# Kernel optimization log

Hardware: AMD Instinct MI355X
Metric: run time of the kernel (lower is better)

Reference implementation:

```python
import jax, jax.numpy as jnp
import numpy as np

EDGE_DROPOUT_RATE = 0.5  # RGCNEncoder edge_dropout_rate
DROPOUT_KEY = 42         # fixed key standing in for the encoder's dropout_key


def setup_inputs() -> dict:
    key = jax.random.key(0)
    ks = jax.random.split(key, 6)
    N, R, E, D, B, BI, BO = 100000, 16, 50000, 500, 100, 5, 5
    x = 0.01 * jax.random.normal(ks[0], (N, D), dtype=jnp.float32)  # pre_transform, normal() init (stddev=0.01)
    # block-decomposed relation weights: R relations x 100 blocks of 5x5
    w_rel1 = jax.random.normal(ks[1], (R, B, BI, BO), dtype=jnp.float32) / np.sqrt(BI)
    w_self1 = jax.random.normal(ks[2], (D, D), dtype=jnp.float32) / np.sqrt(D)
    w_rel2 = jax.random.normal(ks[3], (R, B, BI, BO), dtype=jnp.float32) / np.sqrt(BI)
    w_self2 = jax.random.normal(ks[4], (D, D), dtype=jnp.float32) / np.sqrt(D)
    edge_type_idcs = jax.random.randint(ks[5], (R, 2, E), 0, N, dtype=jnp.int32)
    edge_masks = jnp.ones((R, E), dtype=bool)
    return {"x": x, "w_rel1": w_rel1, "w_self1": w_self1,
            "w_rel2": w_rel2, "w_self2": w_self2,
            "edge_type_idcs": edge_type_idcs, "edge_masks": edge_masks}


def _rgcn_layer(h, w_rel, w_self, edge_type_idcs, edge_mask_f):
    """One block-decomposed RGCNConv with per-relation-node normalization + self loop."""
    N = h.shape[0]
    R, B, BI, BO = w_rel.shape
    Dout = B * BO
    out = h @ w_self  # self-connection
    for r in range(R):  # small fixed set of relations
        src = edge_type_idcs[r, 0]
        dst = edge_type_idcs[r, 1]
        mr = edge_mask_f[r]                              # [E]
        E = src.shape[0]
        hs = h[src].reshape(E, B, BI)                    # gather + split into blocks
        msg = jnp.einsum('ebi,bio->ebo', hs, w_rel[r]).reshape(E, Dout)
        msg = msg * mr[:, None]                          # masked (incl. edge dropout)
        agg = jax.ops.segment_sum(msg, dst, num_segments=N)   # [N, Dout]
        cnt = jax.ops.segment_sum(mr, dst, num_segments=N)    # per-relation in-degree
        out = out + agg / jnp.maximum(cnt, 1.0)[:, None]
    return jax.nn.relu(out)


def reference(x, w_rel1, w_self1, w_rel2, w_self2, edge_type_idcs, edge_masks):
    # edge dropout (all_data.dropout): keep each edge with prob 1 - rate
    keep = jax.random.bernoulli(jax.random.key(DROPOUT_KEY), 1.0 - EDGE_DROPOUT_RATE, edge_masks.shape)
    mask_f = (edge_masks & keep).astype(x.dtype)
    h = _rgcn_layer(x, w_rel1, w_self1, edge_type_idcs, mask_f)
    h = _rgcn_layer(h, w_rel2, w_self2, edge_type_idcs, mask_f)
    return h
```

## Files before the change

kernel.cpp:

```cpp
#include <hip/hip_runtime.h>
#include <hip/hip_bf16.h>
#include <stdint.h>

#define N_NODES 100000
#define N_REL   16
#define N_EDGE  50000
#define DIM     500
#define TOT_E   (N_REL * N_EDGE)
#define CNT_N   (N_REL * N_NODES)

#define INV_OFF    0ull
#define DEG_OFF    6400000ull
#define ROW_OFF    6800000ull
#define SCANP_OFF  7201000ull
#define CURS_OFF   7210000ull
#define ELIST_OFF  7610000ull
#define WB1_OFF    14020000ull
#define WB2_OFF    14550000ull
#define H1_OFF     15080000ull
#define WEXP1_OFF  115080000ull
#define WEXP2_OFF  115240000ull

typedef __attribute__((ext_vector_type(8))) short bf16x8;
typedef __attribute__((ext_vector_type(4))) float f32x4;

__device__ __forceinline__ uint32_t rotl32(uint32_t x, int d) {
    return (x << d) | (x >> (32 - d));
}
__device__ __forceinline__ bool edge_keep(uint32_t j) {
    uint32_t x0 = 0u, x1 = j;
    const uint32_t ks0 = 0u, ks1 = 42u, ks2 = 0u ^ 42u ^ 0x1BD11BDAu;
    const int RA[4] = {13, 15, 26, 6};
    const int RB[4] = {17, 29, 16, 24};
    x0 += ks0; x1 += ks1;
#pragma unroll
    for (int i = 0; i < 4; i++) { x0 += x1; x1 = rotl32(x1, RA[i]); x1 ^= x0; }
    x0 += ks1; x1 += ks2 + 1u;
#pragma unroll
    for (int i = 0; i < 4; i++) { x0 += x1; x1 = rotl32(x1, RB[i]); x1 ^= x0; }
    x0 += ks2; x1 += ks0 + 2u;
#pragma unroll
    for (int i = 0; i < 4; i++) { x0 += x1; x1 = rotl32(x1, RA[i]); x1 ^= x0; }
    x0 += ks0; x1 += ks1 + 3u;
#pragma unroll
    for (int i = 0; i < 4; i++) { x0 += x1; x1 = rotl32(x1, RB[i]); x1 ^= x0; }
    x0 += ks1; x1 += ks2 + 4u;
#pragma unroll
    for (int i = 0; i < 4; i++) { x0 += x1; x1 = rotl32(x1, RA[i]); x1 ^= x0; }
    x0 += ks2; x1 += ks0 + 5u;
    return ((x0 ^ x1) >> 31) == 0u;
}

__device__ __forceinline__ uint16_t f2bf(float f) {
    uint32_t u = __float_as_uint(f);
    u += 0x7FFFu + ((u >> 16) & 1u);
    return (uint16_t)(u >> 16);
}
__device__ __forceinline__ float bf2f(uint16_t v) {
    return __uint_as_float((uint32_t)v << 16);
}

__global__ __launch_bounds__(256) void zero_kernel(uint32_t* __restrict__ p, int n) {
    int t = blockIdx.x * blockDim.x + threadIdx.x;
    if (t < n) p[t] = 0u;
}

__global__ __launch_bounds__(256) void count_kernel(
        const int* __restrict__ eidx, uint32_t* __restrict__ cnt,
        uint32_t* __restrict__ deg) {
    int tid = blockIdx.x * blockDim.x + threadIdx.x;
    if (tid >= TOT_E) return;
    if (edge_keep((uint32_t)tid)) {
        int r = tid / N_EDGE;
        int e = tid - r * N_EDGE;
        int dst = eidx[(r * 2 + 1) * N_EDGE + e];
        atomicAdd(&cnt[r * N_NODES + dst], 1u);
        atomicAdd(&deg[dst], 1u);
    }
}

__global__ __launch_bounds__(256) void inv_kernel(uint32_t* __restrict__ cnt_u,
                                                  float* __restrict__ inv) {
    int t = blockIdx.x * blockDim.x + threadIdx.x;
    if (t < CNT_N) {
        float c = (float)cnt_u[t];
        inv[t] = 1.0f / fmaxf(c, 1.0f);
    }
}

__global__ __launch_bounds__(256) void scan1_kernel(
        const uint32_t* __restrict__ deg, uint32_t* __restrict__ rowptr,
        uint32_t* __restrict__ scanp) {
    __shared__ uint32_t sh[256];
    int b = blockIdx.x, t = threadIdx.x;
    int base = b * 1024 + t * 4;
    uint32_t x[4];
#pragma unroll
    for (int i = 0; i < 4; i++) x[i] = (base + i < N_NODES) ? deg[base + i] : 0u;
    uint32_t s = x[0] + x[1] + x[2] + x[3];
    sh[t] = s; __syncthreads();
    for (int off = 1; off < 256; off <<= 1) {
        uint32_t v = (t >= off) ? sh[t - off] : 0u;
        __syncthreads();
        sh[t] += v;
        __syncthreads();
    }
    uint32_t run = sh[t] - s;
    if (t == 255) scanp[b] = sh[255];
#pragma unroll
    for (int i = 0; i < 4; i++) {
        if (base + i < N_NODES) rowptr[base + i] = run;
        run += x[i];
    }
}

__global__ __launch_bounds__(128) void scan2_kernel(
        uint32_t* __restrict__ scanp, uint32_t* __restrict__ rowptr, int nb) {
    __shared__ uint32_t sh[128];
    int t = threadIdx.x;
    uint32_t v = (t < nb) ? scanp[t] : 0u;
    sh[t] = v; __syncthreads();
    for (int off = 1; off < 128; off <<= 1) {
        uint32_t u = (t >= off) ? sh[t - off] : 0u;
        __syncthreads();
        sh[t] += u;
        __syncthreads();
    }
    if (t < nb) scanp[t] = sh[t] - v;
    if (t == 127) rowptr[N_NODES] = sh[127];
}

__global__ __launch_bounds__(256) void scan3_kernel(
        uint32_t* __restrict__ rowptr, const uint32_t* __restrict__ scanp,
        uint32_t* __restrict__ curs) {
    int b = blockIdx.x, t = threadIdx.x;
    int base = b * 1024 + t * 4;
    uint32_t off = scanp[b];
#pragma unroll
    for (int i = 0; i < 4; i++) {
        int idx = base + i;
        if (idx < N_NODES) {
            uint32_t v = rowptr[idx] + off;
            rowptr[idx] = v;
            curs[idx] = v;
        }
    }
}

__global__ __launch_bounds__(256) void scatter_kernel(
        const int* __restrict__ eidx, const float* __restrict__ inv,
        uint32_t* __restrict__ curs, uint2* __restrict__ elist2) {
    int tid = blockIdx.x * blockDim.x + threadIdx.x;
    if (tid >= TOT_E) return;
    if (edge_keep((uint32_t)tid)) {
        int r = tid / N_EDGE;
        int e = tid - r * N_EDGE;
        int src = eidx[(r * 2 + 0) * N_EDGE + e];
        int dst = eidx[(r * 2 + 1) * N_EDGE + e];
        uint32_t pos = atomicAdd(&curs[dst], 1u);
        uint2 rec;
        rec.x = (uint32_t)src | ((uint32_t)r << 20);
        rec.y = __float_as_uint(inv[r * N_NODES + dst]);
        elist2[pos] = rec;
    }
}

__global__ __launch_bounds__(256) void conv_x_kernel(
        const float4* __restrict__ in, ushort4* __restrict__ outp, int n4) {
    int t = blockIdx.x * blockDim.x + threadIdx.x;
    if (t >= n4) return;
    float4 v = in[t];
    ushort4 o;
    o.x = f2bf(v.x); o.y = f2bf(v.y); o.z = f2bf(v.z); o.w = f2bf(v.w);
    outp[t] = o;
}

__global__ __launch_bounds__(256) void conv_w_kernel(
        const float* __restrict__ W, uint16_t* __restrict__ Bt) {
    int idx = blockIdx.x * 256 + threadIdx.x;
    int n = idx >> 9, k = idx & 511;
    float v = (n < DIM && k < DIM) ? W[k * DIM + n] : 0.f;
    Bt[idx] = f2bf(v);
}

__global__ __launch_bounds__(256) void conv_wexp_kernel(
        const float* __restrict__ W, float* __restrict__ wexp) {
    int idx = blockIdx.x * 256 + threadIdx.x;
    if (idx >= N_REL * 5 * DIM) return;
    int r = idx / (5 * DIM);
    int rem = idx - r * 5 * DIM;
    int i = rem / DIM;
    int j = rem - i * DIM;
    wexp[idx] = W[r * 2500 + (j / 5) * 25 + i * 5 + (j % 5)];
}

__global__ __launch_bounds__(256) void gemm_mfma128_kernel(
        const uint16_t* __restrict__ A, const uint16_t* __restrict__ Bt,
        float* __restrict__ C, int M) {
    __shared__ uint16_t As[128][72];
    __shared__ uint16_t Bs[128][72];
    int m0 = blockIdx.x * 128;
    int n0 = blockIdx.y * 128;
    int t = threadIdx.x;
    int wave = t >> 6, lane = t & 63;
    int wm = wave >> 1, wn = wave & 1;
    f32x4 acc[4][4] = {};

    for (int k0 = 0; k0 < 512; k0 += 64) {
#pragma unroll
        for (int i = 0; i < 4; i++) {
            int c = t * 4 + i;
            int row = c >> 3;
            int col = (c & 7) * 8;
            int gm = m0 + row, gk = k0 + col;
            uint16_t* dst = &As[row][col];
            if (gm < M && gk + 7 < DIM) {
                *(bf16x8*)dst = *(const bf16x8*)&A[(size_t)gm * DIM + gk];
            } else {
#pragma unroll
                for (int q = 0; q < 8; q++)
                    dst[q] = (gm < M && gk + q < DIM) ? A[(size_t)gm * DIM + gk + q]
                                                      : (uint16_t)0;
            }
            *(bf16x8*)&Bs[row][col] =
                *(const bf16x8*)&Bt[(size_t)(n0 + row) * 512 + k0 + col];
        }
        __syncthreads();

        int ks = (lane >> 4) * 8;
        int rl = lane & 15;
        bf16x8 af[4][2], bfr[4][2];
#pragma unroll
        for (int mt = 0; mt < 4; mt++) {
            af[mt][0] = *(const bf16x8*)&As[wm * 64 + mt * 16 + rl][ks];
            af[mt][1] = *(const bf16x8*)&As[wm * 64 + mt * 16 + rl][32 + ks];
        }
#pragma unroll
        for (int nt = 0; nt < 4; nt++) {
            bfr[nt][0] = *(const bf16x8*)&Bs[wn * 64 + nt * 16 + rl][ks];
            bfr[nt][1] = *(const bf16x8*)&Bs[wn * 64 + nt * 16 + rl][32 + ks];
        }
#pragma unroll
        for (int mt = 0; mt < 4; mt++)
#pragma unroll
            for (int nt = 0; nt < 4; nt++) {
                acc[mt][nt] = __builtin_amdgcn_mfma_f32_16x16x32_bf16(
                    af[mt][0], bfr[nt][0], acc[mt][nt], 0, 0, 0);
                acc[mt][nt] = __builtin_amdgcn_mfma_f32_16x16x32_bf16(
                    af[mt][1], bfr[nt][1], acc[mt][nt], 0, 0, 0);
            }
        __syncthreads();
    }

    int cl = lane & 15;
    int rq = (lane >> 4) << 2;
#pragma unroll
    for (int mt = 0; mt < 4; mt++) {
        int rbase = m0 + wm * 64 + mt * 16 + rq;
#pragma unroll
        for (int nt = 0; nt < 4; nt++) {
            int col = n0 + wn * 64 + nt * 16 + cl;
            if (col < DIM) {
#pragma unroll
                for (int q = 0; q < 4; q++) {
                    int rr = rbase + q;
                    if (rr < M) C[(size_t)rr * DIM + col] = acc[mt][nt][q];
                }
            }
        }
    }
}

template <bool BF16H, bool OUT_BF16>
__global__ __launch_bounds__(256) void gather_kernel(
        const void* __restrict__ h, const float* __restrict__ wexp,
        const uint2* __restrict__ elist2, const uint32_t* __restrict__ rowptr,
        const float* __restrict__ self_in, float* __restrict__ out_f32,
        uint16_t* __restrict__ out_bf16) {
    int n = blockIdx.x;
    int wv = threadIdx.x >> 6, l = threadIdx.x & 63;
    const int D0 = wv * 125;
    const int j0 = l, j1 = l + 64;
    const bool has1 = (j1 < 125);
    const int b0 = j0 / 5;
    const int b1 = j1 / 5;

    __shared__ float hsb[4][2][128];

    long ob = (long)n * DIM + D0;
    float self0 = self_in[ob + j0];
    float self1 = has1 ? self_in[ob + j1] : 0.f;

    uint32_t s = rowptr[n], e = rowptr[n + 1];
    float a0 = 0.f, a1 = 0.f;

    for (uint32_t p = s; p < e; p += 4) {
        const int k = (int)min(4u, e - p);
        uint2 rec[4];
#pragma unroll
        for (int i = 0; i < 4; i++) {
            if (i < k) rec[i] = elist2[p + i];
        }
        float v0[4], v1[4];
#pragma unroll
        for (int i = 0; i < 4; i++) {
            if (i < k) {
                uint32_t src = rec[i].x & 0xFFFFFu;
                if constexpr (BF16H) {
                    const uint16_t* row = (const uint16_t*)h + (size_t)src * DIM + D0;
                    v0[i] = bf2f(row[j0]);
                    v1[i] = has1 ? bf2f(row[j1]) : 0.f;
                } else {
                    const float* row = (const float*)h + (size_t)src * DIM + D0;
                    v0[i] = row[j0];
                    v1[i] = has1 ? row[j1] : 0.f;
                }
            }
        }
#pragma unroll
        for (int i = 0; i < 4; i++) {
            if (i < k) {
                float* hs = hsb[wv][i & 1];
                hs[j0] = v0[i];
                if (has1) hs[j1] = v1[i];
                uint32_t rl = rec[i].x >> 20;
                float inv = __uint_as_float(rec[i].y);
                const float* wbase = wexp + (size_t)rl * (5 * DIM) + D0;
                float w0[5];
#pragma unroll
                for (int q = 0; q < 5; q++) w0[q] = wbase[q * DIM + j0];
                const float* hp0 = hs + b0 * 5;
                float d0 = hp0[0] * w0[0] + hp0[1] * w0[1] + hp0[2] * w0[2]
                         + hp0[3] * w0[3] + hp0[4] * w0[4];
                a0 = fmaf(inv, d0, a0);
                if (has1) {
                    float w1[5];
#pragma unroll
                    for (int q = 0; q < 5; q++) w1[q] = wbase[q * DIM + j1];
                    const float* hp1 = hs + b1 * 5;
                    float d1 = hp1[0] * w1[0] + hp1[1] * w1[1] + hp1[2] * w1[2]
                             + hp1[3] * w1[3] + hp1[4] * w1[4];
                    a1 = fmaf(inv, d1, a1);
                }
            }
        }
    }

    {
        float v = fmaxf(self0 + a0, 0.f);
        if (OUT_BF16) out_bf16[ob + j0] = f2bf(v);
        else          out_f32[ob + j0] = v;
    }
    if (has1) {
        float v = fmaxf(self1 + a1, 0.f);
        if (OUT_BF16) out_bf16[ob + j1] = f2bf(v);
        else          out_f32[ob + j1] = v;
    }
}

extern "C" void kernel_launch(void* const* d_in, const int* in_sizes, int n_in,
                              void* d_out, int out_size, void* d_ws, size_t ws_size,
                              hipStream_t stream) {
    const float* x       = nullptr;
    const float* w_rel1  = nullptr;
    const float* w_rel2  = nullptr;
    const float* w_self1 = nullptr;
    const float* w_self2 = nullptr;
    const int*   eidx    = nullptr;
    for (int i = 0; i < n_in; i++) {
        int s = in_sizes[i];
        if (s == N_NODES * DIM) {
            x = (const float*)d_in[i];
        } else if (s == N_REL * 100 * 25) {
            if (!w_rel1) w_rel1 = (const float*)d_in[i];
            else         w_rel2 = (const float*)d_in[i];
        } else if (s == DIM * DIM) {
            if (!w_self1) w_self1 = (const float*)d_in[i];
            else          w_self2 = (const float*)d_in[i];
        } else if (s == N_REL * 2 * N_EDGE) {
            eidx = (const int*)d_in[i];
        }
    }
    float* out = (float*)d_out;

    char* ws = (char*)d_ws;
    uint32_t* cnt_u  = (uint32_t*)(ws + INV_OFF);
    float*    inv    = (float*)(ws + INV_OFF);
    uint32_t* deg    = (uint32_t*)(ws + DEG_OFF);
    uint32_t* rowptr = (uint32_t*)(ws + ROW_OFF);
    uint32_t* scanp  = (uint32_t*)(ws + SCANP_OFF);
    uint32_t* curs   = (uint32_t*)(ws + CURS_OFF);
    uint2*    elist2 = (uint2*)(ws + ELIST_OFF);
    uint16_t* wb1    = (uint16_t*)(ws + WB1_OFF);
    uint16_t* wb2    = (uint16_t*)(ws + WB2_OFF);
    uint16_t* h1     = (uint16_t*)(ws + H1_OFF);
    float*    wexp1  = (float*)(ws + WEXP1_OFF);
    float*    wexp2  = (float*)(ws + WEXP2_OFF);

    const int NB = (N_NODES + 1023) / 1024;

    zero_kernel<<<(CNT_N + N_NODES + 255) / 256, 256, 0, stream>>>(cnt_u, CNT_N + N_NODES);
    count_kernel<<<(TOT_E + 255) / 256, 256, 0, stream>>>(eidx, cnt_u, deg);
    inv_kernel<<<(CNT_N + 255) / 256, 256, 0, stream>>>(cnt_u, inv);
    scan1_kernel<<<NB, 256, 0, stream>>>(deg, rowptr, scanp);
    scan2_kernel<<<1, 128, 0, stream>>>(scanp, rowptr, NB);
    scan3_kernel<<<NB, 256, 0, stream>>>(rowptr, scanp, curs);
    scatter_kernel<<<(TOT_E + 255) / 256, 256, 0, stream>>>(eidx, inv, curs, elist2);

    conv_x_kernel<<<(N_NODES * DIM / 4 + 255) / 256, 256, 0, stream>>>(
        (const float4*)x, (ushort4*)h1, N_NODES * DIM / 4);
    conv_w_kernel<<<512 * 512 / 256, 256, 0, stream>>>(w_self1, wb1);
    conv_w_kernel<<<512 * 512 / 256, 256, 0, stream>>>(w_self2, wb2);
    conv_wexp_kernel<<<(N_REL * 5 * DIM + 255) / 256, 256, 0, stream>>>(w_rel1, wexp1);
    conv_wexp_kernel<<<(N_REL * 5 * DIM + 255) / 256, 256, 0, stream>>>(w_rel2, wexp2);

    dim3 ggrid((N_NODES + 127) / 128, 4);

    gemm_mfma128_kernel<<<ggrid, 256, 0, stream>>>(h1, wb1, out, N_NODES);
    gather_kernel<false, true><<<N_NODES, 256, 0, stream>>>(
        x, wexp1, elist2, rowptr, out, nullptr, h1);

    gemm_mfma128_kernel<<<ggrid, 256, 0, stream>>>(h1, wb2, out, N_NODES);
    gather_kernel<true, false><<<N_NODES, 256, 0, stream>>>(
        h1, wexp2, elist2, rowptr, out, out, nullptr);
}
```

Baseline: 1.202 ms.

## Reorder gather before GEMM and fuse fp32 conversion and ReLU epilogue

```diff
diff --git a/kernel.cpp b/kernel.cpp
--- a/kernel.cpp
+++ b/kernel.cpp
@@ -165,16 +165,6 @@
     }
 }
 
-__global__ __launch_bounds__(256) void conv_x_kernel(
-        const float4* __restrict__ in, ushort4* __restrict__ outp, int n4) {
-    int t = blockIdx.x * blockDim.x + threadIdx.x;
-    if (t >= n4) return;
-    float4 v = in[t];
-    ushort4 o;
-    o.x = f2bf(v.x); o.y = f2bf(v.y); o.z = f2bf(v.z); o.w = f2bf(v.w);
-    outp[t] = o;
-}
-
 __global__ __launch_bounds__(256) void conv_w_kernel(
         const float* __restrict__ W, uint16_t* __restrict__ Bt) {
     int idx = blockIdx.x * 256 + threadIdx.x;
@@ -194,9 +184,10 @@
     wexp[idx] = W[r * 2500 + (j / 5) * 25 + i * 5 + (j % 5)];
 }
 
-__global__ __launch_bounds__(256) void gemm_mfma128_kernel(
-        const uint16_t* __restrict__ A, const uint16_t* __restrict__ Bt,
-        float* __restrict__ C, int M) {
+template <bool AF32, bool OUTBF16>
+__global__ __launch_bounds__(256) void gemm_fused_kernel(
+        const void* __restrict__ A, const uint16_t* __restrict__ Bt,
+        const float* msg, float* outf, uint16_t* houtf, int M) {
     __shared__ uint16_t As[128][72];
     __shared__ uint16_t Bs[128][72];
     int m0 = blockIdx.x * 128;
@@ -214,13 +205,31 @@
             int col = (c & 7) * 8;
             int gm = m0 + row, gk = k0 + col;
             uint16_t* dst = &As[row][col];
-            if (gm < M && gk + 7 < DIM) {
-                *(bf16x8*)dst = *(const bf16x8*)&A[(size_t)gm * DIM + gk];
+            if constexpr (AF32) {
+                const float* Af = (const float*)A;
+                if (gm < M && gk + 7 < DIM) {
+                    float4 p0 = *(const float4*)&Af[(size_t)gm * DIM + gk];
+                    float4 p1 = *(const float4*)&Af[(size_t)gm * DIM + gk + 4];
+                    dst[0] = f2bf(p0.x); dst[1] = f2bf(p0.y);
+                    dst[2] = f2bf(p0.z); dst[3] = f2bf(p0.w);
+                    dst[4] = f2bf(p1.x); dst[5] = f2bf(p1.y);
+                    dst[6] = f2bf(p1.z); dst[7] = f2bf(p1.w);
+                } else {
+#pragma unroll
+                    for (int q = 0; q < 8; q++)
+                        dst[q] = (gm < M && gk + q < DIM)
+                                     ? f2bf(Af[(size_t)gm * DIM + gk + q]) : (uint16_t)0;
+                }
             } else {
-#pragma unroll
-                for (int q = 0; q < 8; q++)
-                    dst[q] = (gm < M && gk + q < DIM) ? A[(size_t)gm * DIM + gk + q]
-                                                      : (uint16_t)0;
+                const uint16_t* Ab = (const uint16_t*)A;
+                if (gm < M && gk + 7 < DIM) {
+                    *(bf16x8*)dst = *(const bf16x8*)&Ab[(size_t)gm * DIM + gk];
+                } else {
+#pragma unroll
+                    for (int q = 0; q < 8; q++)
+                        dst[q] = (gm < M && gk + q < DIM) ? Ab[(size_t)gm * DIM + gk + q]
+                                                          : (uint16_t)0;
+                }
             }
             *(bf16x8*)&Bs[row][col] =
                 *(const bf16x8*)&Bt[(size_t)(n0 + row) * 512 + k0 + col];
@@ -264,19 +273,24 @@
 #pragma unroll
                 for (int q = 0; q < 4; q++) {
                     int rr = rbase + q;
-                    if (rr < M) C[(size_t)rr * DIM + col] = acc[mt][nt][q];
+                    if (rr < M) {
+                        size_t idx = (size_t)rr * DIM + col;
+                        float v = acc[mt][nt][q] + msg[idx];
+                        v = fmaxf(v, 0.f);
+                        if (OUTBF16) houtf[idx] = f2bf(v);
+                        else         outf[idx] = v;
+                    }
                 }
             }
         }
     }
 }
 
-template <bool BF16H, bool OUT_BF16>
-__global__ __launch_bounds__(256) void gather_kernel(
+template <bool BF16H>
+__global__ __launch_bounds__(256) void gather_msg_kernel(
         const void* __restrict__ h, const float* __restrict__ wexp,
         const uint2* __restrict__ elist2, const uint32_t* __restrict__ rowptr,
-        const float* __restrict__ self_in, float* __restrict__ out_f32,
-        uint16_t* __restrict__ out_bf16) {
+        float* __restrict__ msgsum) {
     int n = blockIdx.x;
     int wv = threadIdx.x >> 6, l = threadIdx.x & 63;
     const int D0 = wv * 125;
@@ -286,10 +300,6 @@
     const int b1 = j1 / 5;
 
     __shared__ float hsb[4][2][128];
-
-    long ob = (long)n * DIM + D0;
-    float self0 = self_in[ob + j0];
-    float self1 = has1 ? self_in[ob + j1] : 0.f;
 
     uint32_t s = rowptr[n], e = rowptr[n + 1];
     float a0 = 0.f, a1 = 0.f;
@@ -346,16 +356,9 @@
         }
     }
 
-    {
-        float v = fmaxf(self0 + a0, 0.f);
-        if (OUT_BF16) out_bf16[ob + j0] = f2bf(v);
-        else          out_f32[ob + j0] = v;
-    }
-    if (has1) {
-        float v = fmaxf(self1 + a1, 0.f);
-        if (OUT_BF16) out_bf16[ob + j1] = f2bf(v);
-        else          out_f32[ob + j1] = v;
-    }
+    long ob = (long)n * DIM + D0;
+    msgsum[ob + j0] = a0;
+    if (has1) msgsum[ob + j1] = a1;
 }
 
 extern "C" void kernel_launch(void* const* d_in, const int* in_sizes, int n_in,
@@ -407,8 +410,6 @@
     scan3_kernel<<<NB, 256, 0, stream>>>(rowptr, scanp, curs);
     scatter_kernel<<<(TOT_E + 255) / 256, 256, 0, stream>>>(eidx, inv, curs, elist2);
 
-    conv_x_kernel<<<(N_NODES * DIM / 4 + 255) / 256, 256, 0, stream>>>(
-        (const float4*)x, (ushort4*)h1, N_NODES * DIM / 4);
     conv_w_kernel<<<512 * 512 / 256, 256, 0, stream>>>(w_self1, wb1);
     conv_w_kernel<<<512 * 512 / 256, 256, 0, stream>>>(w_self2, wb2);
     conv_wexp_kernel<<<(N_REL * 5 * DIM + 255) / 256, 256, 0, stream>>>(w_rel1, wexp1);
@@ -416,11 +417,13 @@
 
     dim3 ggrid((N_NODES + 127) / 128, 4);
 
-    gemm_mfma128_kernel<<<ggrid, 256, 0, stream>>>(h1, wb1, out, N_NODES);
-    gather_kernel<false, true><<<N_NODES, 256, 0, stream>>>(
-        x, wexp1, elist2, rowptr, out, nullptr, h1);
-
-    gemm_mfma128_kernel<<<ggrid, 256, 0, stream>>>(h1, wb2, out, N_NODES);
-    gather_kernel<true, false><<<N_NODES, 256, 0, stream>>>(
-        h1, wexp2, elist2, rowptr, out, out, nullptr);
-}
+    gather_msg_kernel<false><<<N_NODES, 256, 0, stream>>>(
+        x, wexp1, elist2, rowptr, out);
+    gemm_fused_kernel<true, true><<<ggrid, 256, 0, stream>>>(
+        x, wb1, out, nullptr, h1, N_NODES);
+
+    gather_msg_kernel<true><<<N_NODES, 256, 0, stream>>>(
+        h1, wexp2, elist2, rowptr, out);
+    gemm_fused_kernel<false, false><<<ggrid, 256, 0, stream>>>(
+        h1, wb2, out, out, nullptr, N_NODES);
+}
```

Result: slower. 1.555 ms (+29.4%).

## Fuse fp32-to-bf16 input conversion into first GEMM and remap blocks per XCD

Applied to the files above, without the earlier changes.

```diff
diff --git a/kernel.cpp b/kernel.cpp
--- a/kernel.cpp
+++ b/kernel.cpp
@@ -165,16 +165,6 @@
     }
 }
 
-__global__ __launch_bounds__(256) void conv_x_kernel(
-        const float4* __restrict__ in, ushort4* __restrict__ outp, int n4) {
-    int t = blockIdx.x * blockDim.x + threadIdx.x;
-    if (t >= n4) return;
-    float4 v = in[t];
-    ushort4 o;
-    o.x = f2bf(v.x); o.y = f2bf(v.y); o.z = f2bf(v.z); o.w = f2bf(v.w);
-    outp[t] = o;
-}
-
 __global__ __launch_bounds__(256) void conv_w_kernel(
         const float* __restrict__ W, uint16_t* __restrict__ Bt) {
     int idx = blockIdx.x * 256 + threadIdx.x;
@@ -194,13 +184,22 @@
     wexp[idx] = W[r * 2500 + (j / 5) * 25 + i * 5 + (j % 5)];
 }
 
+template <bool AF32>
 __global__ __launch_bounds__(256) void gemm_mfma128_kernel(
-        const uint16_t* __restrict__ A, const uint16_t* __restrict__ Bt,
+        const void* __restrict__ A, const uint16_t* __restrict__ Bt,
         float* __restrict__ C, int M) {
+    int bid = blockIdx.x;
+    int xcd = bid & 7;
+    int slot = bid >> 3;
+    int nblk = slot & 3;
+    int mloc = slot >> 2;
+    int mblk = mloc * 8 + xcd;
+    if (mblk >= (N_NODES + 127) / 128) return;
+    int m0 = mblk * 128;
+    int n0 = nblk * 128;
+
     __shared__ uint16_t As[128][72];
     __shared__ uint16_t Bs[128][72];
-    int m0 = blockIdx.x * 128;
-    int n0 = blockIdx.y * 128;
     int t = threadIdx.x;
     int wave = t >> 6, lane = t & 63;
     int wm = wave >> 1, wn = wave & 1;
@@ -214,13 +213,31 @@
             int col = (c & 7) * 8;
             int gm = m0 + row, gk = k0 + col;
             uint16_t* dst = &As[row][col];
-            if (gm < M && gk + 7 < DIM) {
-                *(bf16x8*)dst = *(const bf16x8*)&A[(size_t)gm * DIM + gk];
+            if constexpr (AF32) {
+                const float* Af = (const float*)A;
+                if (gm < M && gk + 7 < DIM) {
+                    float4 p0 = *(const float4*)&Af[(size_t)gm * DIM + gk];
+                    float4 p1 = *(const float4*)&Af[(size_t)gm * DIM + gk + 4];
+                    dst[0] = f2bf(p0.x); dst[1] = f2bf(p0.y);
+                    dst[2] = f2bf(p0.z); dst[3] = f2bf(p0.w);
+                    dst[4] = f2bf(p1.x); dst[5] = f2bf(p1.y);
+                    dst[6] = f2bf(p1.z); dst[7] = f2bf(p1.w);
+                } else {
+#pragma unroll
+                    for (int q = 0; q < 8; q++)
+                        dst[q] = (gm < M && gk + q < DIM)
+                                     ? f2bf(Af[(size_t)gm * DIM + gk + q]) : (uint16_t)0;
+                }
             } else {
-#pragma unroll
-                for (int q = 0; q < 8; q++)
-                    dst[q] = (gm < M && gk + q < DIM) ? A[(size_t)gm * DIM + gk + q]
-                                                      : (uint16_t)0;
+                const uint16_t* Ab = (const uint16_t*)A;
+                if (gm < M && gk + 7 < DIM) {
+                    *(bf16x8*)dst = *(const bf16x8*)&Ab[(size_t)gm * DIM + gk];
+                } else {
+#pragma unroll
+                    for (int q = 0; q < 8; q++)
+                        dst[q] = (gm < M && gk + q < DIM) ? Ab[(size_t)gm * DIM + gk + q]
+                                                          : (uint16_t)0;
+                }
             }
             *(bf16x8*)&Bs[row][col] =
                 *(const bf16x8*)&Bt[(size_t)(n0 + row) * 512 + k0 + col];
@@ -407,20 +424,18 @@
     scan3_kernel<<<NB, 256, 0, stream>>>(rowptr, scanp, curs);
     scatter_kernel<<<(TOT_E + 255) / 256, 256, 0, stream>>>(eidx, inv, curs, elist2);
 
-    conv_x_kernel<<<(N_NODES * DIM / 4 + 255) / 256, 256, 0, stream>>>(
-        (const float4*)x, (ushort4*)h1, N_NODES * DIM / 4);
     conv_w_kernel<<<512 * 512 / 256, 256, 0, stream>>>(w_self1, wb1);
     conv_w_kernel<<<512 * 512 / 256, 256, 0, stream>>>(w_self2, wb2);
     conv_wexp_kernel<<<(N_REL * 5 * DIM + 255) / 256, 256, 0, stream>>>(w_rel1, wexp1);
     conv_wexp_kernel<<<(N_REL * 5 * DIM + 255) / 256, 256, 0, stream>>>(w_rel2, wexp2);
 
-    dim3 ggrid((N_NODES + 127) / 128, 4);
-
-    gemm_mfma128_kernel<<<ggrid, 256, 0, stream>>>(h1, wb1, out, N_NODES);
+    const int GB = 98 * 8 * 4;
+
+    gemm_mfma128_kernel<true><<<GB, 256, 0, stream>>>(x, wb1, out, N_NODES);
     gather_kernel<false, true><<<N_NODES, 256, 0, stream>>>(
         x, wexp1, elist2, rowptr, out, nullptr, h1);
 
-    gemm_mfma128_kernel<<<ggrid, 256, 0, stream>>>(h1, wb2, out, N_NODES);
+    gemm_mfma128_kernel<false><<<GB, 256, 0, stream>>>(h1, wb2, out, N_NODES);
     gather_kernel<true, false><<<N_NODES, 256, 0, stream>>>(
         h1, wexp2, elist2, rowptr, out, out, nullptr);
 }
```

After: 1.226 ms. 1.02x slower.

## Remap GEMM blocks across XCDs and process two nodes per gather block

Applied to the files above, without the earlier changes.

```diff
diff --git a/kernel.cpp b/kernel.cpp
--- a/kernel.cpp
+++ b/kernel.cpp
@@ -197,10 +197,18 @@
 __global__ __launch_bounds__(256) void gemm_mfma128_kernel(
         const uint16_t* __restrict__ A, const uint16_t* __restrict__ Bt,
         float* __restrict__ C, int M) {
+    int bid = blockIdx.x;
+    int xcd = bid & 7;
+    int slot = bid >> 3;
+    int nblk = slot & 3;
+    int mloc = slot >> 2;
+    int mblk = mloc * 8 + xcd;
+    if (mblk >= (N_NODES + 127) / 128) return;
+    int m0 = mblk * 128;
+    int n0 = nblk * 128;
+
     __shared__ uint16_t As[128][72];
     __shared__ uint16_t Bs[128][72];
-    int m0 = blockIdx.x * 128;
-    int n0 = blockIdx.y * 128;
     int t = threadIdx.x;
     int wave = t >> 6, lane = t & 63;
     int wm = wave >> 1, wn = wave & 1;
@@ -277,7 +285,8 @@
         const uint2* __restrict__ elist2, const uint32_t* __restrict__ rowptr,
         const float* __restrict__ self_in, float* __restrict__ out_f32,
         uint16_t* __restrict__ out_bf16) {
-    int n = blockIdx.x;
+    int n0 = blockIdx.x * 2;
+    int n1 = n0 + 1;
     int wv = threadIdx.x >> 6, l = threadIdx.x & 63;
     const int D0 = wv * 125;
     const int j0 = l, j1 = l + 64;
@@ -286,75 +295,138 @@
     const int b1 = j1 / 5;
 
     __shared__ float hsb[4][2][128];
-
-    long ob = (long)n * DIM + D0;
-    float self0 = self_in[ob + j0];
-    float self1 = has1 ? self_in[ob + j1] : 0.f;
-
-    uint32_t s = rowptr[n], e = rowptr[n + 1];
-    float a0 = 0.f, a1 = 0.f;
-
-    for (uint32_t p = s; p < e; p += 4) {
-        const int k = (int)min(4u, e - p);
-        uint2 rec[4];
+    float* hsA = hsb[wv][0];
+    float* hsB = hsb[wv][1];
+
+    long obA = (long)n0 * DIM + D0;
+    long obB = (long)n1 * DIM + D0;
+    float selfA0 = self_in[obA + j0];
+    float selfA1 = has1 ? self_in[obA + j1] : 0.f;
+    float selfB0 = self_in[obB + j0];
+    float selfB1 = has1 ? self_in[obB + j1] : 0.f;
+
+    uint32_t pA = rowptr[n0], eA = rowptr[n0 + 1];
+    uint32_t pB = rowptr[n1], eB = rowptr[n1 + 1];
+    float aA0 = 0.f, aA1 = 0.f, aB0 = 0.f, aB1 = 0.f;
+
+    while (pA < eA || pB < eB) {
+        const int kA = (int)min(4u, eA - pA);
+        const int kB = (int)min(4u, eB - pB);
+
+        uint2 recA[4], recB[4];
+#pragma unroll
+        for (int i = 0; i < 4; i++) { if (i < kA) recA[i] = elist2[pA + i]; }
+#pragma unroll
+        for (int i = 0; i < 4; i++) { if (i < kB) recB[i] = elist2[pB + i]; }
+
+        float vA0[4], vA1[4], vB0[4], vB1[4];
 #pragma unroll
         for (int i = 0; i < 4; i++) {
-            if (i < k) rec[i] = elist2[p + i];
-        }
-        float v0[4], v1[4];
-#pragma unroll
-        for (int i = 0; i < 4; i++) {
-            if (i < k) {
-                uint32_t src = rec[i].x & 0xFFFFFu;
+            if (i < kA) {
+                uint32_t src = recA[i].x & 0xFFFFFu;
                 if constexpr (BF16H) {
                     const uint16_t* row = (const uint16_t*)h + (size_t)src * DIM + D0;
-                    v0[i] = bf2f(row[j0]);
-                    v1[i] = has1 ? bf2f(row[j1]) : 0.f;
+                    vA0[i] = bf2f(row[j0]);
+                    vA1[i] = has1 ? bf2f(row[j1]) : 0.f;
                 } else {
                     const float* row = (const float*)h + (size_t)src * DIM + D0;
-                    v0[i] = row[j0];
-                    v1[i] = has1 ? row[j1] : 0.f;
+                    vA0[i] = row[j0];
+                    vA1[i] = has1 ? row[j1] : 0.f;
                 }
             }
         }
 #pragma unroll
         for (int i = 0; i < 4; i++) {
-            if (i < k) {
-                float* hs = hsb[wv][i & 1];
-                hs[j0] = v0[i];
-                if (has1) hs[j1] = v1[i];
-                uint32_t rl = rec[i].x >> 20;
-                float inv = __uint_as_float(rec[i].y);
+            if (i < kB) {
+                uint32_t src = recB[i].x & 0xFFFFFu;
+                if constexpr (BF16H) {
+                    const uint16_t* row = (const uint16_t*)h + (size_t)src * DIM + D0;
+                    vB0[i] = bf2f(row[j0]);
+                    vB1[i] = has1 ? bf2f(row[j1]) : 0.f;
+                } else {
+                    const float* row = (const float*)h + (size_t)src * DIM + D0;
+                    vB0[i] = row[j0];
+                    vB1[i] = has1 ? row[j1] : 0.f;
+                }
+            }
+        }
+
+#pragma unroll
+        for (int i = 0; i < 4; i++) {
+            if (i < kA) {
+                hsA[j0] = vA0[i];
+                if (has1) hsA[j1] = vA1[i];
+                uint32_t rl = recA[i].x >> 20;
+                float inv = __uint_as_float(recA[i].y);
                 const float* wbase = wexp + (size_t)rl * (5 * DIM) + D0;
                 float w0[5];
 #pragma unroll
                 for (int q = 0; q < 5; q++) w0[q] = wbase[q * DIM + j0];
-                const float* hp0 = hs + b0 * 5;
+                const float* hp0 = hsA + b0 * 5;
                 float d0 = hp0[0] * w0[0] + hp0[1] * w0[1] + hp0[2] * w0[2]
                          + hp0[3] * w0[3] + hp0[4] * w0[4];
-                a0 = fmaf(inv, d0, a0);
+                aA0 = fmaf(inv, d0, aA0);
                 if (has1) {
                     float w1[5];
 #pragma unroll
                     for (int q = 0; q < 5; q++) w1[q] = wbase[q * DIM + j1];
-                    const float* hp1 = hs + b1 * 5;
+                    const float* hp1 = hsA + b1 * 5;
                     float d1 = hp1[0] * w1[0] + hp1[1] * w1[1] + hp1[2] * w1[2]
                              + hp1[3] * w1[3] + hp1[4] * w1[4];
-                    a1 = fmaf(inv, d1, a1);
+                    aA1 = fmaf(inv, d1, aA1);
                 }
             }
         }
+#pragma unroll
+        for (int i = 0; i < 4; i++) {
+            if (i < kB) {
+                hsB[j0] = vB0[i];
+                if (has1) hsB[j1] = vB1[i];
+                uint32_t rl = recB[i].x >> 20;
+                float inv = __uint_as_float(recB[i].y);
+                const float* wbase = wexp + (size_t)rl * (5 * DIM) + D0;
+                float w0[5];
+#pragma unroll
+                for (int q = 0; q < 5; q++) w0[q] = wbase[q * DIM + j0];
+                const float* hp0 = hsB + b0 * 5;
+                float d0 = hp0[0] * w0[0] + hp0[1] * w0[1] + hp0[2] * w0[2]
+                         + hp0[3] * w0[3] + hp0[4] * w0[4];
+                aB0 = fmaf(inv, d0, aB0);
+                if (has1) {
+                    float w1[5];
+#pragma unroll
+                    for (int q = 0; q < 5; q++) w1[q] = wbase[q * DIM + j1];
+                    const float* hp1 = hsB + b1 * 5;
+                    float d1 = hp1[0] * w1[0] + hp1[1] * w1[1] + hp1[2] * w1[2]
+                             + hp1[3] * w1[3] + hp1[4] * w1[4];
+                    aB1 = fmaf(inv, d1, aB1);
+                }
+            }
+        }
+
+        pA += kA;
+        pB += kB;
     }
 
     {
-        float v = fmaxf(self0 + a0, 0.f);
-        if (OUT_BF16) out_bf16[ob + j0] = f2bf(v);
-        else          out_f32[ob + j0] = v;
+        float v = fmaxf(selfA0 + aA0, 0.f);
+        if (OUT_BF16) out_bf16[obA + j0] = f2bf(v);
+        else          out_f32[obA + j0] = v;
     }
     if (has1) {
-        float v = fmaxf(self1 + a1, 0.f);
-        if (OUT_BF16) out_bf16[ob + j1] = f2bf(v);
-        else          out_f32[ob + j1] = v;
+        float v = fmaxf(selfA1 + aA1, 0.f);
+        if (OUT_BF16) out_bf16[obA + j1] = f2bf(v);
+        else          out_f32[obA + j1] = v;
+    }
+    {
+        float v = fmaxf(selfB0 + aB0, 0.f);
+        if (OUT_BF16) out_bf16[obB + j0] = f2bf(v);
+        else          out_f32[obB + j0] = v;
+    }
+    if (has1) {
+        float v = fmaxf(selfB1 + aB1, 0.f);
+        if (OUT_BF16) out_bf16[obB + j1] = f2bf(v);
+        else          out_f32[obB + j1] = v;
     }
 }
 
@@ -414,13 +486,13 @@
     conv_wexp_kernel<<<(N_REL * 5 * DIM + 255) / 256, 256, 0, stream>>>(w_rel1, wexp1);
     conv_wexp_kernel<<<(N_REL * 5 * DIM + 255) / 256, 256, 0, stream>>>(w_rel2, wexp2);
 
-    dim3 ggrid((N_NODES + 127) / 128, 4);
-
-    gemm_mfma128_kernel<<<ggrid, 256, 0, stream>>>(h1, wb1, out, N_NODES);
-    gather_kernel<false, true><<<N_NODES, 256, 0, stream>>>(
+    const int GB = 98 * 8 * 4;
+
+    gemm_mfma128_kernel<<<GB, 256, 0, stream>>>(h1, wb1, out, N_NODES);
+    gather_kernel<false, true><<<N_NODES / 2, 256, 0, stream>>>(
         x, wexp1, elist2, rowptr, out, nullptr, h1);
 
-    gemm_mfma128_kernel<<<ggrid, 256, 0, stream>>>(h1, wb2, out, N_NODES);
-    gather_kernel<true, false><<<N_NODES, 256, 0, stream>>>(
+    gemm_mfma128_kernel<<<GB, 256, 0, stream>>>(h1, wb2, out, N_NODES);
+    gather_kernel<true, false><<<N_NODES / 2, 256, 0, stream>>>(
         h1, wexp2, elist2, rowptr, out, out, nullptr);
 }
```

After: 1.186 ms. About the same (-1.3%).
